# Optimization experiments

Measured on AMD Instinct MI355X. Metric: run time of the kernel, lower is better.

Reference implementation:

```python
import jax, jax.numpy as jnp
import numpy as np

N, E, G = 50000, 500000, 64
F_IN, H, C = 10, 4, 64
HC = H * C  # 256
NCLS = 8
BN_EPS = 1e-5


def _bn(x, g, b, m, v):
    # eval-mode BatchNorm1d with running stats
    return (x - m) * jax.lax.rsqrt(v + BN_EPS) * g + b


def _gat(x, src, dst, W, a_s, a_d, b):
    # PyG GATConv (concat=True): h=[N,H,C]; e_ij=leakyrelu(a_s.h_j + a_d.h_i);
    # softmax over incoming edges of each destination node; scatter-add.
    n = x.shape[0]
    h = (x @ W).reshape(n, H, C)
    es = jnp.einsum('nhc,hc->nh', h, a_s)  # source term per node
    ed = jnp.einsum('nhc,hc->nh', h, a_d)  # dest term per node
    e = jax.nn.leaky_relu(es[src] + ed[dst], 0.2)            # [E2,H]
    m = jax.ops.segment_max(e, dst, num_segments=n)
    ex = jnp.exp(e - m[dst])
    s = jax.ops.segment_sum(ex, dst, num_segments=n)
    alpha = ex / (s[dst] + 1e-16)                             # [E2,H]
    out = jax.ops.segment_sum(h[src] * alpha[:, :, None], dst, num_segments=n)
    return out.reshape(n, HC) + b, alpha


def _gcn(x, src, dst, W, b):
    n = x.shape[0]
    deg = jax.ops.segment_sum(jnp.ones_like(src, dtype=x.dtype), dst, num_segments=n)
    dinv = jax.lax.rsqrt(jnp.maximum(deg, 1.0))
    norm = dinv[src] * dinv[dst]
    xw = x @ W
    return jax.ops.segment_sum(xw[src] * norm[:, None], dst, num_segments=n) + b


def setup_inputs() -> dict:
    key = jax.random.key(0)
    ks = jax.random.split(key, 48)
    r = lambda i, sh, sc=0.1: jax.random.normal(ks[i], sh, dtype=jnp.float32) * sc
    p = {}
    p['x'] = jax.random.normal(ks[0], (N, F_IN), dtype=jnp.float32)
    p['edge_index'] = jax.random.randint(ks[1], (2, E), 0, N, dtype=jnp.int32)
    p['batch'] = jnp.sort(jax.random.randint(ks[2], (N,), 0, G, dtype=jnp.int32))
    # GAT1
    p['W1'] = r(3, (F_IN, HC)); p['as1'] = r(4, (H, C)); p['ad1'] = r(5, (H, C)); p['bi1'] = r(6, (HC,))
    # GAT2
    p['W2'] = r(7, (HC, HC)); p['as2'] = r(8, (H, C)); p['ad2'] = r(9, (H, C)); p['bi2'] = r(10, (HC,))
    # BN running stats / affine
    for i, (nm, d) in enumerate([('bn1', HC), ('bn2', HC), ('bn3', C)]):
        k0 = 11 + 4 * i
        p[nm + '_g'] = 1.0 + r(k0, (d,))
        p[nm + '_b'] = r(k0 + 1, (d,))
        p[nm + '_m'] = r(k0 + 2, (d,))
        p[nm + '_v'] = 1.0 + jax.random.uniform(ks[k0 + 3], (d,), dtype=jnp.float32) * 0.5
    # GCN
    p['Wg'] = r(23, (HC, C)); p['bg'] = r(24, (C,))
    # reduce_dim
    p['Wr'] = r(25, (2 * C, C)); p['br'] = r(26, (C,))
    # rul head
    p['Wh1'] = r(27, (C, 32)); p['bh1'] = r(28, (32,))
    p['Wh2'] = r(29, (32, 16)); p['bh2'] = r(30, (16,))
    p['Wh3'] = r(31, (16, 1)); p['bh3'] = r(32, (1,))
    # location head
    p['Wl1'] = r(33, (C, 32)); p['bl1'] = r(34, (32,))
    p['Wl2'] = r(35, (32, NCLS)); p['bl2'] = r(36, (NCLS,))
    # energy head
    p['We1'] = r(37, (C, 16)); p['be1'] = r(38, (16,))
    p['We2'] = r(39, (16, 1)); p['be2'] = r(40, (1,))
    return p


def reference(x, edge_index, batch,
              W1, as1, ad1, bi1, W2, as2, ad2, bi2,
              bn1_g, bn1_b, bn1_m, bn1_v, bn2_g, bn2_b, bn2_m, bn2_v,
              bn3_g, bn3_b, bn3_m, bn3_v,
              Wg, bg, Wr, br,
              Wh1, bh1, Wh2, bh2, Wh3, bh3,
              Wl1, bl1, Wl2, bl2, We1, be1, We2, be2):
    n = x.shape[0]
    loop = jnp.arange(n, dtype=edge_index.dtype)
    src = jnp.concatenate([edge_index[0], loop])
    dst = jnp.concatenate([edge_index[1], loop])

    h, alpha1 = _gat(x, src, dst, W1, as1, ad1, bi1)
    h = jax.nn.elu(_bn(h, bn1_g, bn1_b, bn1_m, bn1_v))  # dropout = identity (eval)
    h, alpha2 = _gat(h, src, dst, W2, as2, ad2, bi2)
    h = jax.nn.elu(_bn(h, bn2_g, bn2_b, bn2_m, bn2_v))
    h = _gcn(h, src, dst, Wg, bg)
    h = jax.nn.elu(_bn(h, bn3_g, bn3_b, bn3_m, bn3_v))  # node embeddings [N,64]

    cnt = jax.ops.segment_sum(jnp.ones((n,), h.dtype), batch, num_segments=G)
    x_mean = jax.ops.segment_sum(h, batch, num_segments=G) / jnp.maximum(cnt, 1.0)[:, None]
    x_max = jax.ops.segment_max(h, batch, num_segments=G)
    x_max = jnp.where(cnt[:, None] > 0, x_max, 0.0)
    xg = jnp.concatenate([x_mean, x_max], axis=1) @ Wr + br  # [G,64]

    t = jax.nn.relu(xg @ Wh1 + bh1)
    t = jax.nn.relu(t @ Wh2 + bh2)
    rul = jax.nn.sigmoid(t @ Wh3 + bh3) * 100.0
    loc = jax.nn.relu(xg @ Wl1 + bl1) @ Wl2 + bl2
    en = jax.nn.relu(xg @ We1 + be1) @ We2 + be2
    return rul, loc, en, h, xg
```

## Files before the change

### kernel.cpp

```cpp
#include <hip/hip_runtime.h>
#include <math.h>

#define SCAN_BLK 1024
#define BN_EPS 1e-5f

typedef __attribute__((ext_vector_type(8))) short short8;
typedef __attribute__((ext_vector_type(4))) short short4v;
typedef __attribute__((ext_vector_type(4))) float f32x4;

__device__ __forceinline__ float eluf(float x){ return x > 0.f ? x : (expf(x) - 1.f); }
__device__ __forceinline__ unsigned short f2bf(float f){
  unsigned u = __float_as_uint(f);
  u += 0x7FFFu + ((u >> 16) & 1u);
  return (unsigned short)(u >> 16);
}
__device__ __forceinline__ float bf2f(unsigned short s){
  return __uint_as_float(((unsigned)s) << 16);
}
__device__ __forceinline__ unsigned fmap(float f){
  unsigned b = __float_as_uint(f);
  return (b & 0x80000000u) ? ~b : (b | 0x80000000u);
}
__device__ __forceinline__ float funmap(unsigned u){
  unsigned b = (u & 0x80000000u) ? (u ^ 0x80000000u) : ~u;
  return __uint_as_float(b);
}

__global__ void k_count(const int* __restrict__ ei, int* __restrict__ deg, int ne, int e2)
{
  int t = blockIdx.x * 256 + threadIdx.x;
  if (t >= e2) return;
  int dst = (t < ne) ? ei[ne + t] : t - ne;
  atomicAdd(&deg[dst], 1);
}

__global__ void k_scan1(const int* __restrict__ deg, int* __restrict__ rowptr,
                        int* __restrict__ partials, int n)
{
  __shared__ int sh[SCAN_BLK];
  int t = threadIdx.x, base = blockIdx.x * SCAN_BLK;
  int v = (base + t < n) ? deg[base + t] : 0;
  sh[t] = v;
  __syncthreads();
  for (int off = 1; off < SCAN_BLK; off <<= 1) {
    int u = 0;
    if (t >= off) u = sh[t - off];
    __syncthreads();
    if (t >= off) sh[t] += u;
    __syncthreads();
  }
  if (base + t < n) rowptr[base + t] = sh[t] - v;
  if (t == SCAN_BLK - 1) partials[blockIdx.x] = sh[t];
}

__global__ void k_scan2(int* __restrict__ rowptr, const int* __restrict__ partials, int n)
{
  int base = blockIdx.x * SCAN_BLK;
  int add = 0;
  for (int i = 0; i < blockIdx.x; i++) add += partials[i];
  int t = threadIdx.x;
  if (base + t < n) rowptr[base + t] += add;
}

__global__ void k_fill(const int* __restrict__ ei, const int* __restrict__ rowptr,
                       int* __restrict__ cursor, int* __restrict__ col, int ne, int e2)
{
  int t = blockIdx.x * 256 + threadIdx.x;
  if (t >= e2) return;
  int src, dst;
  if (t < ne) { src = ei[t]; dst = ei[ne + t]; } else { src = dst = t - ne; }
  int pos = rowptr[dst] + atomicAdd(&cursor[dst], 1);
  col[pos] = src;
}

__global__ void k_dinv(const int* __restrict__ deg, float* __restrict__ dinv, int n)
{
  int t = blockIdx.x * 256 + threadIdx.x;
  if (t < n) dinv[t] = rsqrtf(fmaxf((float)deg[t], 1.f));
}

__global__ void k_pack(const float* __restrict__ W, unsigned short* __restrict__ Wp,
                       int N, int nct)
{
  int tid = threadIdx.x;
  int l = tid >> 3, j = tid & 7;
  int ct = blockIdx.x >> 3, ks = blockIdx.x & 7;
  int k = ks * 32 + (l >> 4) * 8 + j;
  int c = ct * 16 + (l & 15);
  Wp[(size_t)(ks * nct + ct) * 512 + tid] = f2bf(W[(size_t)k * N + c]);
}

__global__ void k_prep1(const float* __restrict__ W1, const float* __restrict__ as1,
                        const float* __restrict__ ad1,
                        float* __restrict__ Ws1, float* __restrict__ Wd1)
{
  int t = threadIdx.x;
  if (t >= 80) return;
  int half = t / 40, r = t % 40;
  int k = r / 4, h = r % 4;
  const float* a = half ? ad1 : as1;
  float s = 0.f;
  for (int c = 0; c < 64; c++) s += W1[k * 256 + h * 64 + c] * a[h * 64 + c];
  (half ? Wd1 : Ws1)[k * 4 + h] = s;
}

__global__ void k_prep2(const float* __restrict__ W2, const float* __restrict__ as2,
                        const float* __restrict__ ad2,
                        float* __restrict__ Was2, float* __restrict__ Wad2)
{
  int g = blockIdx.x * 256 + threadIdx.x;
  if (g >= 2048) return;
  int half = g >= 1024, r = g & 1023;
  int i = r >> 2, h = r & 3;
  const float* a = half ? ad2 : as2;
  float s = 0.f;
  for (int c = 0; c < 64; c++) s += W2[(size_t)i * 256 + h * 64 + c] * a[h * 64 + c];
  (half ? Wad2 : Was2)[i * 4 + h] = s;
}

__global__ void k_prep_bn(const float* __restrict__ bi1, const float* __restrict__ g1,
                          const float* __restrict__ b1, const float* __restrict__ m1,
                          const float* __restrict__ v1,
                          const float* __restrict__ bi2, const float* __restrict__ g2,
                          const float* __restrict__ b2, const float* __restrict__ m2,
                          const float* __restrict__ v2,
                          float* __restrict__ A1, float* __restrict__ B1,
                          float* __restrict__ A2, float* __restrict__ B2)
{
  int c = threadIdx.x;
  if (c < 256) {
    float a = rsqrtf(v1[c] + BN_EPS) * g1[c];
    A1[c] = a; B1[c] = (bi1[c] - m1[c]) * a + b1[c];
    a = rsqrtf(v2[c] + BN_EPS) * g2[c];
    A2[c] = a; B2[c] = (bi2[c] - m2[c]) * a + b2[c];
  }
}

__global__ void k_es1(const float* __restrict__ x, const float* __restrict__ Ws1,
                      const float* __restrict__ Wd1,
                      float* __restrict__ es, float* __restrict__ ed, int n)
{
  int t = blockIdx.x * 256 + threadIdx.x;
  if (t >= n) return;
  float xr[10];
  #pragma unroll
  for (int k = 0; k < 10; k++) xr[k] = x[(size_t)t * 10 + k];
  float e0[4] = {0,0,0,0}, e1[4] = {0,0,0,0};
  #pragma unroll
  for (int k = 0; k < 10; k++) {
    #pragma unroll
    for (int h = 0; h < 4; h++) {
      e0[h] += xr[k] * Ws1[k * 4 + h];
      e1[h] += xr[k] * Wd1[k * 4 + h];
    }
  }
  *(float4*)&es[t * 4] = make_float4(e0[0], e0[1], e0[2], e0[3]);
  *(float4*)&ed[t * 4] = make_float4(e1[0], e1[1], e1[2], e1[3]);
}

__global__ void k_esed2(const unsigned short* __restrict__ act,
                        const float* __restrict__ Was2, const float* __restrict__ Wad2,
                        float* __restrict__ es, float* __restrict__ ed, int n)
{
  int nn = blockIdx.x * 4 + (threadIdx.x >> 6);
  if (nn >= n) return;
  int lane = threadIdx.x & 63;
  short4v av = *(const short4v*)&act[(size_t)nn * 256 + lane * 4];
  float e0[4] = {0,0,0,0}, e1[4] = {0,0,0,0};
  #pragma unroll
  for (int j = 0; j < 4; j++) {
    int c = lane * 4 + j;
    float v = bf2f((unsigned short)av[j]);
    float4 ws = *(const float4*)&Was2[c * 4];
    float4 wd = *(const float4*)&Wad2[c * 4];
    e0[0] += v * ws.x; e0[1] += v * ws.y; e0[2] += v * ws.z; e0[3] += v * ws.w;
    e1[0] += v * wd.x; e1[1] += v * wd.y; e1[2] += v * wd.z; e1[3] += v * wd.w;
  }
  #pragma unroll
  for (int off = 1; off < 64; off <<= 1) {
    #pragma unroll
    for (int h = 0; h < 4; h++) {
      e0[h] += __shfl_xor(e0[h], off, 64);
      e1[h] += __shfl_xor(e1[h], off, 64);
    }
  }
  if (lane == 0) {
    *(float4*)&es[nn * 4] = make_float4(e0[0], e0[1], e0[2], e0[3]);
    *(float4*)&ed[nn * 4] = make_float4(e1[0], e1[1], e1[2], e1[3]);
  }
}

__global__ void k_att_ms(const int* __restrict__ rowptr, const int* __restrict__ deg,
                         const int* __restrict__ col,
                         const float* __restrict__ es, const float* __restrict__ ed,
                         float* __restrict__ alp, float* __restrict__ sinv, int n)
{
  int d = blockIdx.x * 4 + (threadIdx.x >> 6);
  if (d >= n) return;
  int lane = threadIdx.x & 63;
  int head = lane >> 4, sub = lane & 15;
  int start = rowptr[d], cnt = deg[d];
  float edh = ed[d * 4 + head];

  float m = -1e30f;
  for (int i = sub; i < cnt; i += 16) {
    int s = col[start + i];
    float a = es[s * 4 + head] + edh;
    a = a > 0.f ? a : 0.2f * a;
    m = fmaxf(m, a);
  }
  #pragma unroll
  for (int off = 1; off < 16; off <<= 1) m = fmaxf(m, __shfl_xor(m, off, 16));

  float ssum = 0.f;
  for (int i = sub; i < cnt; i += 16) {
    int s = col[start + i];
    float a = es[s * 4 + head] + edh;
    a = a > 0.f ? a : 0.2f * a;
    float ex = expf(a - m);
    alp[(size_t)(start + i) * 4 + head] = ex;
    ssum += ex;
  }
  #pragma unroll
  for (int off = 1; off < 16; off <<= 1) ssum += __shfl_xor(ssum, off, 16);
  if (sub == 0) sinv[d * 4 + head] = 1.f / (ssum + 1e-16f);
}

__global__ void k_xagg(const int* __restrict__ rowptr, const int* __restrict__ deg,
                       const int* __restrict__ col, const float* __restrict__ alp,
                       const float* __restrict__ sinv, const float* __restrict__ x,
                       float* __restrict__ xa, int n)
{
  int d = blockIdx.x * 4 + (threadIdx.x >> 6);
  if (d >= n) return;
  int lane = threadIdx.x & 63;
  int slot = lane >> 4, k = lane & 15;
  int start = rowptr[d], cnt = deg[d];
  bool active = (k < 10);

  float a0 = 0.f, a1 = 0.f, a2 = 0.f, a3 = 0.f;
  int i = slot;
  for (; i + 4 < cnt; i += 8) {
    int e0 = start + i, e1 = start + i + 4;
    int s0 = col[e0], s1 = col[e1];
    float4 al0 = *(const float4*)&alp[(size_t)e0 * 4];
    float4 al1 = *(const float4*)&alp[(size_t)e1 * 4];
    float x0 = active ? x[(size_t)s0 * 10 + k] : 0.f;
    float x1 = active ? x[(size_t)s1 * 10 + k] : 0.f;
    a0 += al0.x * x0 + al1.x * x1;
    a1 += al0.y * x0 + al1.y * x1;
    a2 += al0.z * x0 + al1.z * x1;
    a3 += al0.w * x0 + al1.w * x1;
  }
  if (i < cnt) {
    int e0 = start + i;
    int s0 = col[e0];
    float4 al0 = *(const float4*)&alp[(size_t)e0 * 4];
    float x0 = active ? x[(size_t)s0 * 10 + k] : 0.f;
    a0 += al0.x * x0; a1 += al0.y * x0; a2 += al0.z * x0; a3 += al0.w * x0;
  }
  a0 += __shfl_xor(a0, 16, 64); a0 += __shfl_xor(a0, 32, 64);
  a1 += __shfl_xor(a1, 16, 64); a1 += __shfl_xor(a1, 32, 64);
  a2 += __shfl_xor(a2, 16, 64); a2 += __shfl_xor(a2, 32, 64);
  a3 += __shfl_xor(a3, 16, 64); a3 += __shfl_xor(a3, 32, 64);

  if (slot == 0 && active) {
    float4 sv = *(const float4*)&sinv[d * 4];
    float* xo = &xa[(size_t)d * 40];
    xo[k]      = a0 * sv.x;
    xo[10 + k] = a1 * sv.y;
    xo[20 + k] = a2 * sv.z;
    xo[30 + k] = a3 * sv.w;
  }
}

__global__ void k_gemm_xa(const float* __restrict__ xa, const float* __restrict__ W1,
                          const float* __restrict__ A1, const float* __restrict__ B1,
                          unsigned short* __restrict__ actA, int n)
{
  __shared__ float xal[160];
  int tid = threadIdx.x;
  int n0 = blockIdx.x * 4;
  if (tid < 160 && (size_t)n0 * 40 + tid < (size_t)n * 40)
    xal[tid] = xa[(size_t)n0 * 40 + tid];
  __syncthreads();
  int c = tid, h = c >> 6;
  float w[10];
  #pragma unroll
  for (int k = 0; k < 10; k++) w[k] = W1[k * 256 + c];
  float a1 = A1[c], b1 = B1[c];
  #pragma unroll
  for (int m = 0; m < 4; m++) {
    int nn = n0 + m;
    if (nn >= n) break;
    float acc = 0.f;
    #pragma unroll
    for (int k = 0; k < 10; k++) acc += xal[m * 40 + h * 10 + k] * w[k];
    actA[(size_t)nn * 256 + c] = f2bf(eluf(acc * a1 + b1));
  }
}

__global__ void k_gat_gather(const int* __restrict__ rowptr, const int* __restrict__ deg,
                             const int* __restrict__ col, const float* __restrict__ alp,
                             const float* __restrict__ sinv,
                             const unsigned short* __restrict__ act,
                             unsigned short* __restrict__ outb, int n)
{
  int d = blockIdx.x * 4 + (threadIdx.x >> 6);
  if (d >= n) return;
  int lane = threadIdx.x & 63;
  int half = lane >> 5, l32 = lane & 31;
  int c8 = l32 * 8, head = l32 >> 3;
  int start = rowptr[d], cnt = deg[d];

  float acc[8] = {0.f,0.f,0.f,0.f,0.f,0.f,0.f,0.f};
  int T = (cnt > half) ? ((cnt - half + 1) >> 1) : 0;
  int ebase = start + half;
  int t = 0;
  for (; t + 4 <= T; t += 4) {
    int e0 = ebase + 2 * t, e1 = e0 + 2, e2 = e0 + 4, e3 = e0 + 6;
    int s0 = col[e0], s1 = col[e1], s2 = col[e2], s3 = col[e3];
    float a0 = alp[(size_t)e0 * 4 + head];
    float a1 = alp[(size_t)e1 * 4 + head];
    float a2 = alp[(size_t)e2 * 4 + head];
    float a3 = alp[(size_t)e3 * 4 + head];
    short8 h0 = *(const short8*)&act[(size_t)s0 * 256 + c8];
    short8 h1 = *(const short8*)&act[(size_t)s1 * 256 + c8];
    short8 h2 = *(const short8*)&act[(size_t)s2 * 256 + c8];
    short8 h3 = *(const short8*)&act[(size_t)s3 * 256 + c8];
    #pragma unroll
    for (int j = 0; j < 8; j++) {
      acc[j] += bf2f((unsigned short)h0[j]) * a0 + bf2f((unsigned short)h1[j]) * a1
              + bf2f((unsigned short)h2[j]) * a2 + bf2f((unsigned short)h3[j]) * a3;
    }
  }
  for (; t < T; t++) {
    int e0 = ebase + 2 * t;
    int s0 = col[e0];
    float a0 = alp[(size_t)e0 * 4 + head];
    short8 h0 = *(const short8*)&act[(size_t)s0 * 256 + c8];
    #pragma unroll
    for (int j = 0; j < 8; j++) acc[j] += bf2f((unsigned short)h0[j]) * a0;
  }
  #pragma unroll
  for (int j = 0; j < 8; j++)
    acc[j] += __shfl_xor(acc[j], 32, 64);

  if (half == 0) {
    float sv = sinv[d * 4 + head];
    short8 o;
    #pragma unroll
    for (int j = 0; j < 8; j++) o[j] = (short)f2bf(acc[j] * sv);
    *(short8*)&outb[(size_t)d * 256 + c8] = o;
  }
}

template<int NCT, bool BNEPI>
__global__ __launch_bounds__(256) void k_mfma_gemm(
    const unsigned short* __restrict__ act, const unsigned short* __restrict__ Wp,
    unsigned short* __restrict__ outb,
    const float* __restrict__ Abn, const float* __restrict__ Bbn, int n)
{
  __shared__ unsigned short bsh[NCT * 512];
  int tid = threadIdx.x, wave = tid >> 6, lane = tid & 63;
  int l15 = lane & 15, lg = lane >> 4;
  int rbase = blockIdx.x * 64 + wave * 16;
  int arow = rbase + l15; if (arow > n - 1) arow = n - 1;
  const unsigned short* ap = &act[(size_t)arow * 256 + lg * 8];

  constexpr int NCH = (NCT >= 4) ? NCT / 4 : 1;
  f32x4 acc[NCT];
  f32x4 z = {0.f, 0.f, 0.f, 0.f};
  #pragma unroll
  for (int ct = 0; ct < NCT; ct++) acc[ct] = z;

  for (int ks = 0; ks < 8; ks++) {
    const unsigned short* src = Wp + (size_t)ks * NCT * 512 + wave * NCT * 128;
    short8 stg[NCH];
    #pragma unroll
    for (int c = 0; c < NCH; c++)
      stg[c] = *(const short8*)(src + c * 512 + lane * 8);
    short8 a = *(const short8*)(ap + ks * 32);
    __syncthreads();
    #pragma unroll
    for (int c = 0; c < NCH; c++)
      *(short8*)&bsh[wave * NCT * 128 + c * 512 + lane * 8] = stg[c];
    __syncthreads();
    #pragma unroll
    for (int ct = 0; ct < NCT; ct++) {
      short8 b = *(const short8*)&bsh[(ct * 64 + lane) * 8];
      acc[ct] = __builtin_amdgcn_mfma_f32_16x16x32_bf16(a, b, acc[ct], 0, 0, 0);
    }
  }

  float abn[NCT], bbn[NCT];
  if (BNEPI) {
    #pragma unroll
    for (int ct = 0; ct < NCT; ct++) {
      abn[ct] = Abn[ct * 16 + l15];
      bbn[ct] = Bbn[ct * 16 + l15];
    }
  }
  #pragma unroll
  for (int r = 0; r < 4; r++) {
    int row = rbase + lg * 4 + r;
    if (row < n) {
      #pragma unroll
      for (int ct = 0; ct < NCT; ct++) {
        float v = acc[ct][r];
        if (BNEPI) v = eluf(v * abn[ct] + bbn[ct]);
        outb[(size_t)row * (NCT * 16) + ct * 16 + l15] = f2bf(v);
      }
    }
  }
}

__global__ void k_gcn_gather(const int* __restrict__ rowptr, const int* __restrict__ deg,
                             const int* __restrict__ col, const float* __restrict__ dinv,
                             const unsigned short* __restrict__ xwb,
                             const float* __restrict__ bias,
                             const float* __restrict__ gg, const float* __restrict__ bb,
                             const float* __restrict__ mm, const float* __restrict__ vv,
                             float* __restrict__ hout, int n)
{
  int d = blockIdx.x * 4 + (threadIdx.x >> 6);
  if (d >= n) return;
  int lane = threadIdx.x & 63;
  int slot = lane >> 3, cg = (lane & 7) * 8;
  int start = rowptr[d], cnt = deg[d];
  float dinvd = rsqrtf(fmaxf((float)cnt, 1.f));

  float acc[8] = {0.f,0.f,0.f,0.f,0.f,0.f,0.f,0.f};
  for (int i = slot; i < cnt; i += 8) {
    int s = col[start + i];
    float norm = dinv[s] * dinvd;
    short8 hv = *(const short8*)&xwb[(size_t)s * 64 + cg];
    #pragma unroll
    for (int j = 0; j < 8; j++)
      acc[j] += bf2f((unsigned short)hv[j]) * norm;
  }
  #pragma unroll
  for (int j = 0; j < 8; j++) {
    acc[j] += __shfl_xor(acc[j], 8, 64);
    acc[j] += __shfl_xor(acc[j], 16, 64);
    acc[j] += __shfl_xor(acc[j], 32, 64);
  }

  if (lane < 8) {
    float out[8];
    #pragma unroll
    for (int j = 0; j < 8; j++) {
      int c = cg + j;
      float r = ((acc[j] + bias[c]) - mm[c]) * rsqrtf(vv[c] + BN_EPS) * gg[c] + bb[c];
      out[j] = eluf(r);
    }
    *(float4*)&hout[(size_t)d * 64 + cg]     = make_float4(out[0], out[1], out[2], out[3]);
    *(float4*)&hout[(size_t)d * 64 + cg + 4] = make_float4(out[4], out[5], out[6], out[7]);
  }
}

__global__ void k_pool_partial(const float* __restrict__ hout, const int* __restrict__ batch,
                               float* __restrict__ psum, unsigned* __restrict__ pmaxu,
                               int n)
{
  int wave = threadIdx.x >> 6, lane = threadIdx.x & 63;
  int wbase = blockIdx.x * 128 + wave * 32;
  int wend = wbase + 32; if (wend > n) wend = n;
  if (wbase >= n) return;

  int g_cur = -1;
  float s = 0.f, mx = -1e30f;
  for (int node = wbase; node < wend; node++) {
    int g = batch[node];
    if (g != g_cur) {
      if (g_cur >= 0) {
        atomicAdd(&psum[g_cur * 64 + lane], s);
        atomicMax(&pmaxu[g_cur * 64 + lane], fmap(mx));
      }
      g_cur = g; s = 0.f; mx = -1e30f;
    }
    float v = hout[(size_t)node * 64 + lane];
    s += v;
    mx = fmaxf(mx, v);
  }
  if (g_cur >= 0) {
    atomicAdd(&psum[g_cur * 64 + lane], s);
    atomicMax(&pmaxu[g_cur * 64 + lane], fmap(mx));
  }
}

__global__ void k_heads(const float* __restrict__ psum, const unsigned* __restrict__ pmaxu,
                        const int* __restrict__ batch,
                        const float* __restrict__ Wr, const float* __restrict__ br,
                        const float* __restrict__ Wh1, const float* __restrict__ bh1,
                        const float* __restrict__ Wh2, const float* __restrict__ bh2,
                        const float* __restrict__ Wh3, const float* __restrict__ bh3,
                        const float* __restrict__ Wl1, const float* __restrict__ bl1,
                        const float* __restrict__ Wl2, const float* __restrict__ bl2,
                        const float* __restrict__ We1, const float* __restrict__ be1,
                        const float* __restrict__ We2, const float* __restrict__ be2,
                        float* __restrict__ outp, int n, int xg_off)
{
  __shared__ float cat[128], xg[64], t1[32], t2[16], l1[32], e1[16];
  int g = blockIdx.x, c = threadIdx.x;

  int lo = 0, hi = n;
  while (lo < hi) { int mid = (lo + hi) >> 1; if (batch[mid] < g) lo = mid + 1; else hi = mid; }
  int start = lo;
  lo = start; hi = n;
  while (lo < hi) { int mid = (lo + hi) >> 1; if (batch[mid] < g + 1) lo = mid + 1; else hi = mid; }
  int cntg = lo - start;

  float mean = psum[g * 64 + c] / fmaxf((float)cntg, 1.f);
  float mxv = (cntg > 0) ? funmap(pmaxu[g * 64 + c]) : 0.f;
  cat[c] = mean; cat[64 + c] = mxv;
  __syncthreads();
  float a = br[c];
  for (int i = 0; i < 128; i++) a += cat[i] * Wr[i * 64 + c];
  xg[c] = a;
  outp[xg_off + g * 64 + c] = a;
  __syncthreads();
  if (c < 32) {
    float u = bh1[c]; for (int i = 0; i < 64; i++) u += xg[i] * Wh1[i * 32 + c];
    t1[c] = fmaxf(u, 0.f);
    float v = bl1[c]; for (int i = 0; i < 64; i++) v += xg[i] * Wl1[i * 32 + c];
    l1[c] = fmaxf(v, 0.f);
  }
  __syncthreads();
  if (c < 16) {
    float u = bh2[c]; for (int i = 0; i < 32; i++) u += t1[i] * Wh2[i * 16 + c];
    t2[c] = fmaxf(u, 0.f);
    float v = be1[c]; for (int i = 0; i < 64; i++) v += xg[i] * We1[i * 16 + c];
    e1[c] = fmaxf(v, 0.f);
  }
  __syncthreads();
  if (c < 8) {
    float v = bl2[c]; for (int i = 0; i < 32; i++) v += l1[i] * Wl2[i * 8 + c];
    outp[64 + g * 8 + c] = v;
  }
  if (c == 0) {
    float u = bh3[0]; for (int i = 0; i < 16; i++) u += t2[i] * Wh3[i];
    outp[g] = 100.f / (1.f + expf(-u));
    float v = be2[0]; for (int i = 0; i < 16; i++) v += e1[i] * We2[i];
    outp[576 + g] = v;
  }
}

extern "C" void kernel_launch(void* const* d_in, const int* in_sizes, int n_in,
                              void* d_out, int out_size, void* d_ws, size_t ws_size,
                              hipStream_t stream)
{
  const float* x    = (const float*)d_in[0];
  const int*   ei   = (const int*)d_in[1];
  const int*   batch= (const int*)d_in[2];
  const float* W1   = (const float*)d_in[3];
  const float* as1  = (const float*)d_in[4];
  const float* ad1  = (const float*)d_in[5];
  const float* bi1  = (const float*)d_in[6];
  const float* W2   = (const float*)d_in[7];
  const float* as2  = (const float*)d_in[8];
  const float* ad2  = (const float*)d_in[9];
  const float* bi2  = (const float*)d_in[10];
  const float* bn1g = (const float*)d_in[11];
  const float* bn1b = (const float*)d_in[12];
  const float* bn1m = (const float*)d_in[13];
  const float* bn1v = (const float*)d_in[14];
  const float* bn2g = (const float*)d_in[15];
  const float* bn2b = (const float*)d_in[16];
  const float* bn2m = (const float*)d_in[17];
  const float* bn2v = (const float*)d_in[18];
  const float* bn3g = (const float*)d_in[19];
  const float* bn3b = (const float*)d_in[20];
  const float* bn3m = (const float*)d_in[21];
  const float* bn3v = (const float*)d_in[22];
  const float* Wg   = (const float*)d_in[23];
  const float* bg   = (const float*)d_in[24];
  const float* Wr   = (const float*)d_in[25];
  const float* br   = (const float*)d_in[26];
  const float* Wh1  = (const float*)d_in[27];
  const float* bh1  = (const float*)d_in[28];
  const float* Wh2  = (const float*)d_in[29];
  const float* bh2  = (const float*)d_in[30];
  const float* Wh3  = (const float*)d_in[31];
  const float* bh3  = (const float*)d_in[32];
  const float* Wl1  = (const float*)d_in[33];
  const float* bl1  = (const float*)d_in[34];
  const float* Wl2  = (const float*)d_in[35];
  const float* bl2  = (const float*)d_in[36];
  const float* We1  = (const float*)d_in[37];
  const float* be1  = (const float*)d_in[38];
  const float* We2  = (const float*)d_in[39];
  const float* be2  = (const float*)d_in[40];

  const int n  = in_sizes[2];
  const int ne = in_sizes[1] / 2;
  const int e2 = ne + n;

  float* ws = (float*)d_ws;
  size_t off = 0;
  unsigned short* bufA = (unsigned short*)(ws + off); off += (size_t)n * 128;
  unsigned short* bufB = (unsigned short*)(ws + off); off += (size_t)n * 128;
  float* xa   = ws + off; off += (size_t)n * 40;
  float* es   = ws + off; off += (size_t)n * 4;
  float* ed   = ws + off; off += (size_t)n * 4;
  float* alp  = ws + off; off += (size_t)e2 * 4;
  float* sinv = ws + off; off += (size_t)n * 4;
  float* dinv = ws + off; off += (size_t)n;
  int* rowptr = (int*)(ws + off); off += (size_t)n + 1;
  int* deg    = (int*)(ws + off); off += (size_t)n;
  int* cursor = (int*)(ws + off); off += (size_t)n;
  int* col    = (int*)(ws + off); off += (size_t)e2;
  int* partials = (int*)(ws + off); off += 64;
  unsigned short* Wp2 = (unsigned short*)(ws + off); off += 32768;
  unsigned short* Wpg = (unsigned short*)(ws + off); off += 8192;
  float* Ws1  = ws + off; off += 40;
  float* Wd1  = ws + off; off += 40;
  float* Was2 = ws + off; off += 1024;
  float* Wad2 = ws + off; off += 1024;
  float* A1   = ws + off; off += 256;
  float* B1   = ws + off; off += 256;
  float* A2   = ws + off; off += 256;
  float* B2   = ws + off; off += 256;
  float* psum = ws + off; off += 64 * 64;
  unsigned* pmaxu = (unsigned*)(ws + off); off += 64 * 64;

  unsigned short* actA = bufA;
  unsigned short* agg2 = bufB;
  unsigned short* actB = bufA;
  unsigned short* xwb  = bufB;

  float* outp = (float*)d_out;
  float* hout = outp + 640;
  const int xg_off = 640 + n * 64;

  const int eb   = (e2 + 255) / 256;
  const int gb1  = (n + 3) / 4;
  const int gmb  = (n + 63) / 64;
  const int nsb  = (n + SCAN_BLK - 1) / SCAN_BLK;

  hipMemsetAsync(deg, 0, (size_t)n * sizeof(int), stream);
  hipMemsetAsync(cursor, 0, (size_t)n * sizeof(int), stream);
  k_count<<<eb, 256, 0, stream>>>(ei, deg, ne, e2);
  k_scan1<<<nsb, SCAN_BLK, 0, stream>>>(deg, rowptr, partials, n);
  k_scan2<<<nsb, SCAN_BLK, 0, stream>>>(rowptr, partials, n);
  k_fill<<<eb, 256, 0, stream>>>(ei, rowptr, cursor, col, ne, e2);
  k_dinv<<<(n + 255) / 256, 256, 0, stream>>>(deg, dinv, n);
  k_pack<<<128, 512, 0, stream>>>(W2, Wp2, 256, 16);
  k_pack<<<32, 512, 0, stream>>>(Wg, Wpg, 64, 4);
  k_prep1<<<1, 128, 0, stream>>>(W1, as1, ad1, Ws1, Wd1);
  k_prep2<<<8, 256, 0, stream>>>(W2, as2, ad2, Was2, Wad2);
  k_prep_bn<<<1, 256, 0, stream>>>(bi1, bn1g, bn1b, bn1m, bn1v,
                                   bi2, bn2g, bn2b, bn2m, bn2v,
                                   A1, B1, A2, B2);

  k_es1<<<(n + 255) / 256, 256, 0, stream>>>(x, Ws1, Wd1, es, ed, n);
  k_att_ms<<<gb1, 256, 0, stream>>>(rowptr, deg, col, es, ed, alp, sinv, n);
  k_xagg<<<gb1, 256, 0, stream>>>(rowptr, deg, col, alp, sinv, x, xa, n);
  k_gemm_xa<<<gb1, 256, 0, stream>>>(xa, W1, A1, B1, actA, n);

  k_esed2<<<gb1, 256, 0, stream>>>(actA, Was2, Wad2, es, ed, n);
  k_att_ms<<<gb1, 256, 0, stream>>>(rowptr, deg, col, es, ed, alp, sinv, n);
  k_gat_gather<<<gb1, 256, 0, stream>>>(rowptr, deg, col, alp, sinv, actA, agg2, n);
  k_mfma_gemm<16, true><<<gmb, 256, 0, stream>>>(agg2, Wp2, actB, A2, B2, n);

  k_mfma_gemm<4, false><<<gmb, 256, 0, stream>>>(actB, Wpg, xwb, nullptr, nullptr, n);
  k_gcn_gather<<<gb1, 256, 0, stream>>>(rowptr, deg, col, dinv, xwb,
                                        bg, bn3g, bn3b, bn3m, bn3v, hout, n);

  hipMemsetAsync(psum, 0, 64 * 64 * sizeof(float), stream);
  hipMemsetAsync(pmaxu, 0, 64 * 64 * sizeof(unsigned), stream);
  k_pool_partial<<<(n + 127) / 128, 256, 0, stream>>>(hout, batch, psum, pmaxu, n);
  k_heads<<<64, 64, 0, stream>>>(psum, pmaxu, batch, Wr, br,
                                 Wh1, bh1, Wh2, bh2, Wh3, bh3,
                                 Wl1, bl1, Wl2, bl2, We1, be1, We2, be2,
                                 outp, n, xg_off);
}
```

Baseline: 342.6 us.

## Fuse attention softmax into gather kernels, drop max subtraction and alpha buffer

Removes the separate attention kernel that computed per-edge exponentials and inverse sums. Both GAT aggregation kernels now recompute exp(leakyrelu(es+ed)) inline and accumulate the normalising sum themselves. This removes a full edge pass and the per-edge alpha write and read. The softmax no longer subtracts the per-destination max, which risks overflow when logits are large. The esed2 kernel is also restructured to 8 threads per node with transposed weights, and the GCN gather is unrolled by two with dinv[dst] hoisted out of the loop.

```diff
diff --git a/kernel.cpp b/kernel.cpp
--- a/kernel.cpp
+++ b/kernel.cpp
@@ -25,6 +25,7 @@
   unsigned b = (u & 0x80000000u) ? (u ^ 0x80000000u) : ~u;
   return __uint_as_float(b);
 }
+__device__ __forceinline__ float lrelu(float a){ return a > 0.f ? a : 0.2f * a; }
 
 __global__ void k_count(const int* __restrict__ ei, int* __restrict__ deg, int ne, int e2)
 {
@@ -105,8 +106,7 @@
 }
 
 __global__ void k_prep2(const float* __restrict__ W2, const float* __restrict__ as2,
-                        const float* __restrict__ ad2,
-                        float* __restrict__ Was2, float* __restrict__ Wad2)
+                        const float* __restrict__ ad2, float* __restrict__ WasT)
 {
   int g = blockIdx.x * 256 + threadIdx.x;
   if (g >= 2048) return;
@@ -115,7 +115,7 @@
   const float* a = half ? ad2 : as2;
   float s = 0.f;
   for (int c = 0; c < 64; c++) s += W2[(size_t)i * 256 + h * 64 + c] * a[h * 64 + c];
-  (half ? Wad2 : Was2)[i * 4 + h] = s;
+  WasT[(size_t)(half * 4 + h) * 256 + i] = s;
 }
 
 __global__ void k_prep_bn(const float* __restrict__ bi1, const float* __restrict__ g1,
@@ -159,77 +159,33 @@
 }
 
 __global__ void k_esed2(const unsigned short* __restrict__ act,
-                        const float* __restrict__ Was2, const float* __restrict__ Wad2,
+                        const float* __restrict__ WasT,
                         float* __restrict__ es, float* __restrict__ ed, int n)
 {
-  int nn = blockIdx.x * 4 + (threadIdx.x >> 6);
+  int t = blockIdx.x * 256 + threadIdx.x;
+  int nn = t >> 3, q = t & 7;
   if (nn >= n) return;
-  int lane = threadIdx.x & 63;
-  short4v av = *(const short4v*)&act[(size_t)nn * 256 + lane * 4];
-  float e0[4] = {0,0,0,0}, e1[4] = {0,0,0,0};
-  #pragma unroll
-  for (int j = 0; j < 4; j++) {
-    int c = lane * 4 + j;
-    float v = bf2f((unsigned short)av[j]);
-    float4 ws = *(const float4*)&Was2[c * 4];
-    float4 wd = *(const float4*)&Wad2[c * 4];
-    e0[0] += v * ws.x; e0[1] += v * ws.y; e0[2] += v * ws.z; e0[3] += v * ws.w;
-    e1[0] += v * wd.x; e1[1] += v * wd.y; e1[2] += v * wd.z; e1[3] += v * wd.w;
-  }
-  #pragma unroll
-  for (int off = 1; off < 64; off <<= 1) {
-    #pragma unroll
-    for (int h = 0; h < 4; h++) {
-      e0[h] += __shfl_xor(e0[h], off, 64);
-      e1[h] += __shfl_xor(e1[h], off, 64);
-    }
-  }
-  if (lane == 0) {
-    *(float4*)&es[nn * 4] = make_float4(e0[0], e0[1], e0[2], e0[3]);
-    *(float4*)&ed[nn * 4] = make_float4(e1[0], e1[1], e1[2], e1[3]);
-  }
-}
-
-__global__ void k_att_ms(const int* __restrict__ rowptr, const int* __restrict__ deg,
-                         const int* __restrict__ col,
-                         const float* __restrict__ es, const float* __restrict__ ed,
-                         float* __restrict__ alp, float* __restrict__ sinv, int n)
-{
-  int d = blockIdx.x * 4 + (threadIdx.x >> 6);
-  if (d >= n) return;
-  int lane = threadIdx.x & 63;
-  int head = lane >> 4, sub = lane & 15;
-  int start = rowptr[d], cnt = deg[d];
-  float edh = ed[d * 4 + head];
-
-  float m = -1e30f;
-  for (int i = sub; i < cnt; i += 16) {
-    int s = col[start + i];
-    float a = es[s * 4 + head] + edh;
-    a = a > 0.f ? a : 0.2f * a;
-    m = fmaxf(m, a);
-  }
-  #pragma unroll
-  for (int off = 1; off < 16; off <<= 1) m = fmaxf(m, __shfl_xor(m, off, 16));
-
-  float ssum = 0.f;
-  for (int i = sub; i < cnt; i += 16) {
-    int s = col[start + i];
-    float a = es[s * 4 + head] + edh;
-    a = a > 0.f ? a : 0.2f * a;
-    float ex = expf(a - m);
-    alp[(size_t)(start + i) * 4 + head] = ex;
-    ssum += ex;
-  }
-  #pragma unroll
-  for (int off = 1; off < 16; off <<= 1) ssum += __shfl_xor(ssum, off, 16);
-  if (sub == 0) sinv[d * 4 + head] = 1.f / (ssum + 1e-16f);
+  const unsigned short* ar = &act[(size_t)nn * 256];
+  const float* wr = &WasT[(size_t)q * 256];
+  float s = 0.f;
+  #pragma unroll 4
+  for (int c0 = 0; c0 < 256; c0 += 8) {
+    short8 av = *(const short8*)(ar + c0);
+    float4 w0 = *(const float4*)(wr + c0);
+    float4 w1 = *(const float4*)(wr + c0 + 4);
+    s += bf2f((unsigned short)av[0]) * w0.x + bf2f((unsigned short)av[1]) * w0.y
+       + bf2f((unsigned short)av[2]) * w0.z + bf2f((unsigned short)av[3]) * w0.w
+       + bf2f((unsigned short)av[4]) * w1.x + bf2f((unsigned short)av[5]) * w1.y
+       + bf2f((unsigned short)av[6]) * w1.z + bf2f((unsigned short)av[7]) * w1.w;
+  }
+  if (q < 4) es[nn * 4 + q] = s;
+  else       ed[nn * 4 + (q - 4)] = s;
 }
 
 __global__ void k_xagg(const int* __restrict__ rowptr, const int* __restrict__ deg,
-                       const int* __restrict__ col, const float* __restrict__ alp,
-                       const float* __restrict__ sinv, const float* __restrict__ x,
-                       float* __restrict__ xa, int n)
+                       const int* __restrict__ col,
+                       const float* __restrict__ es, const float* __restrict__ ed,
+                       const float* __restrict__ x, float* __restrict__ xa, int n)
 {
   int d = blockIdx.x * 4 + (threadIdx.x >> 6);
   if (d >= n) return;
@@ -237,40 +193,54 @@
   int slot = lane >> 4, k = lane & 15;
   int start = rowptr[d], cnt = deg[d];
   bool active = (k < 10);
+  float4 edv = *(const float4*)&ed[d * 4];
 
   float a0 = 0.f, a1 = 0.f, a2 = 0.f, a3 = 0.f;
+  float s0 = 0.f, s1 = 0.f, s2 = 0.f, s3 = 0.f;
   int i = slot;
   for (; i + 4 < cnt; i += 8) {
     int e0 = start + i, e1 = start + i + 4;
-    int s0 = col[e0], s1 = col[e1];
-    float4 al0 = *(const float4*)&alp[(size_t)e0 * 4];
-    float4 al1 = *(const float4*)&alp[(size_t)e1 * 4];
-    float x0 = active ? x[(size_t)s0 * 10 + k] : 0.f;
-    float x1 = active ? x[(size_t)s1 * 10 + k] : 0.f;
-    a0 += al0.x * x0 + al1.x * x1;
-    a1 += al0.y * x0 + al1.y * x1;
-    a2 += al0.z * x0 + al1.z * x1;
-    a3 += al0.w * x0 + al1.w * x1;
+    int sa = col[e0], sb = col[e1];
+    float4 u0 = *(const float4*)&es[sa * 4];
+    float4 u1 = *(const float4*)&es[sb * 4];
+    float x0 = active ? x[(size_t)sa * 10 + k] : 0.f;
+    float x1 = active ? x[(size_t)sb * 10 + k] : 0.f;
+    float ex;
+    ex = expf(lrelu(u0.x + edv.x)); a0 += ex * x0; s0 += ex;
+    ex = expf(lrelu(u0.y + edv.y)); a1 += ex * x0; s1 += ex;
+    ex = expf(lrelu(u0.z + edv.z)); a2 += ex * x0; s2 += ex;
+    ex = expf(lrelu(u0.w + edv.w)); a3 += ex * x0; s3 += ex;
+    ex = expf(lrelu(u1.x + edv.x)); a0 += ex * x1; s0 += ex;
+    ex = expf(lrelu(u1.y + edv.y)); a1 += ex * x1; s1 += ex;
+    ex = expf(lrelu(u1.z + edv.z)); a2 += ex * x1; s2 += ex;
+    ex = expf(lrelu(u1.w + edv.w)); a3 += ex * x1; s3 += ex;
   }
   if (i < cnt) {
     int e0 = start + i;
-    int s0 = col[e0];
-    float4 al0 = *(const float4*)&alp[(size_t)e0 * 4];
-    float x0 = active ? x[(size_t)s0 * 10 + k] : 0.f;
-    a0 += al0.x * x0; a1 += al0.y * x0; a2 += al0.z * x0; a3 += al0.w * x0;
+    int sa = col[e0];
+    float4 u0 = *(const float4*)&es[sa * 4];
+    float x0 = active ? x[(size_t)sa * 10 + k] : 0.f;
+    float ex;
+    ex = expf(lrelu(u0.x + edv.x)); a0 += ex * x0; s0 += ex;
+    ex = expf(lrelu(u0.y + edv.y)); a1 += ex * x0; s1 += ex;
+    ex = expf(lrelu(u0.z + edv.z)); a2 += ex * x0; s2 += ex;
+    ex = expf(lrelu(u0.w + edv.w)); a3 += ex * x0; s3 += ex;
   }
   a0 += __shfl_xor(a0, 16, 64); a0 += __shfl_xor(a0, 32, 64);
   a1 += __shfl_xor(a1, 16, 64); a1 += __shfl_xor(a1, 32, 64);
   a2 += __shfl_xor(a2, 16, 64); a2 += __shfl_xor(a2, 32, 64);
   a3 += __shfl_xor(a3, 16, 64); a3 += __shfl_xor(a3, 32, 64);
+  s0 += __shfl_xor(s0, 16, 64); s0 += __shfl_xor(s0, 32, 64);
+  s1 += __shfl_xor(s1, 16, 64); s1 += __shfl_xor(s1, 32, 64);
+  s2 += __shfl_xor(s2, 16, 64); s2 += __shfl_xor(s2, 32, 64);
+  s3 += __shfl_xor(s3, 16, 64); s3 += __shfl_xor(s3, 32, 64);
 
   if (slot == 0 && active) {
-    float4 sv = *(const float4*)&sinv[d * 4];
     float* xo = &xa[(size_t)d * 40];
-    xo[k]      = a0 * sv.x;
-    xo[10 + k] = a1 * sv.y;
-    xo[20 + k] = a2 * sv.z;
-    xo[30 + k] = a3 * sv.w;
+    xo[k]      = a0 / (s0 + 1e-16f);
+    xo[10 + k] = a1 / (s1 + 1e-16f);
+    xo[20 + k] = a2 / (s2 + 1e-16f);
+    xo[30 + k] = a3 / (s3 + 1e-16f);
   }
 }
 
@@ -301,8 +271,8 @@
 }
 
 __global__ void k_gat_gather(const int* __restrict__ rowptr, const int* __restrict__ deg,
-                             const int* __restrict__ col, const float* __restrict__ alp,
-                             const float* __restrict__ sinv,
+                             const int* __restrict__ col,
+                             const float* __restrict__ es, const float* __restrict__ ed,
                              const unsigned short* __restrict__ act,
                              unsigned short* __restrict__ outb, int n)
 {
@@ -312,42 +282,47 @@
   int half = lane >> 5, l32 = lane & 31;
   int c8 = l32 * 8, head = l32 >> 3;
   int start = rowptr[d], cnt = deg[d];
+  float edh = ed[d * 4 + head];
 
   float acc[8] = {0.f,0.f,0.f,0.f,0.f,0.f,0.f,0.f};
+  float sex = 0.f;
   int T = (cnt > half) ? ((cnt - half + 1) >> 1) : 0;
   int ebase = start + half;
   int t = 0;
   for (; t + 4 <= T; t += 4) {
     int e0 = ebase + 2 * t, e1 = e0 + 2, e2 = e0 + 4, e3 = e0 + 6;
     int s0 = col[e0], s1 = col[e1], s2 = col[e2], s3 = col[e3];
-    float a0 = alp[(size_t)e0 * 4 + head];
-    float a1 = alp[(size_t)e1 * 4 + head];
-    float a2 = alp[(size_t)e2 * 4 + head];
-    float a3 = alp[(size_t)e3 * 4 + head];
+    float x0 = expf(lrelu(es[s0 * 4 + head] + edh));
+    float x1 = expf(lrelu(es[s1 * 4 + head] + edh));
+    float x2 = expf(lrelu(es[s2 * 4 + head] + edh));
+    float x3 = expf(lrelu(es[s3 * 4 + head] + edh));
     short8 h0 = *(const short8*)&act[(size_t)s0 * 256 + c8];
     short8 h1 = *(const short8*)&act[(size_t)s1 * 256 + c8];
     short8 h2 = *(const short8*)&act[(size_t)s2 * 256 + c8];
     short8 h3 = *(const short8*)&act[(size_t)s3 * 256 + c8];
     #pragma unroll
     for (int j = 0; j < 8; j++) {
-      acc[j] += bf2f((unsigned short)h0[j]) * a0 + bf2f((unsigned short)h1[j]) * a1
-              + bf2f((unsigned short)h2[j]) * a2 + bf2f((unsigned short)h3[j]) * a3;
+      acc[j] += bf2f((unsigned short)h0[j]) * x0 + bf2f((unsigned short)h1[j]) * x1
+              + bf2f((unsigned short)h2[j]) * x2 + bf2f((unsigned short)h3[j]) * x3;
     }
+    sex += x0 + x1 + x2 + x3;
   }
   for (; t < T; t++) {
     int e0 = ebase + 2 * t;
     int s0 = col[e0];
-    float a0 = alp[(size_t)e0 * 4 + head];
+    float x0 = expf(lrelu(es[s0 * 4 + head] + edh));
     short8 h0 = *(const short8*)&act[(size_t)s0 * 256 + c8];
     #pragma unroll
-    for (int j = 0; j < 8; j++) acc[j] += bf2f((unsigned short)h0[j]) * a0;
+    for (int j = 0; j < 8; j++) acc[j] += bf2f((unsigned short)h0[j]) * x0;
+    sex += x0;
   }
   #pragma unroll
   for (int j = 0; j < 8; j++)
     acc[j] += __shfl_xor(acc[j], 32, 64);
+  sex += __shfl_xor(sex, 32, 64);
 
   if (half == 0) {
-    float sv = sinv[d * 4 + head];
+    float sv = 1.f / (sex + 1e-16f);
     short8 o;
     #pragma unroll
     for (int j = 0; j < 8; j++) o[j] = (short)f2bf(acc[j] * sv);
@@ -431,19 +406,30 @@
   float dinvd = rsqrtf(fmaxf((float)cnt, 1.f));
 
   float acc[8] = {0.f,0.f,0.f,0.f,0.f,0.f,0.f,0.f};
-  for (int i = slot; i < cnt; i += 8) {
-    int s = col[start + i];
-    float norm = dinv[s] * dinvd;
-    short8 hv = *(const short8*)&xwb[(size_t)s * 64 + cg];
+  int i = slot;
+  for (; i + 8 < cnt; i += 16) {
+    int s0 = col[start + i], s1 = col[start + i + 8];
+    float n0 = dinv[s0], n1 = dinv[s1];
+    short8 h0 = *(const short8*)&xwb[(size_t)s0 * 64 + cg];
+    short8 h1 = *(const short8*)&xwb[(size_t)s1 * 64 + cg];
     #pragma unroll
     for (int j = 0; j < 8; j++)
-      acc[j] += bf2f((unsigned short)hv[j]) * norm;
+      acc[j] += bf2f((unsigned short)h0[j]) * n0 + bf2f((unsigned short)h1[j]) * n1;
+  }
+  if (i < cnt) {
+    int s0 = col[start + i];
+    float n0 = dinv[s0];
+    short8 h0 = *(const short8*)&xwb[(size_t)s0 * 64 + cg];
+    #pragma unroll
+    for (int j = 0; j < 8; j++)
+      acc[j] += bf2f((unsigned short)h0[j]) * n0;
   }
   #pragma unroll
   for (int j = 0; j < 8; j++) {
     acc[j] += __shfl_xor(acc[j], 8, 64);
     acc[j] += __shfl_xor(acc[j], 16, 64);
     acc[j] += __shfl_xor(acc[j], 32, 64);
+    acc[j] *= dinvd;
   }
 
   if (lane < 8) {
@@ -603,8 +589,6 @@
   float* xa   = ws + off; off += (size_t)n * 40;
   float* es   = ws + off; off += (size_t)n * 4;
   float* ed   = ws + off; off += (size_t)n * 4;
-  float* alp  = ws + off; off += (size_t)e2 * 4;
-  float* sinv = ws + off; off += (size_t)n * 4;
   float* dinv = ws + off; off += (size_t)n;
   int* rowptr = (int*)(ws + off); off += (size_t)n + 1;
   int* deg    = (int*)(ws + off); off += (size_t)n;
@@ -615,8 +599,7 @@
   unsigned short* Wpg = (unsigned short*)(ws + off); off += 8192;
   float* Ws1  = ws + off; off += 40;
   float* Wd1  = ws + off; off += 40;
-  float* Was2 = ws + off; off += 1024;
-  float* Wad2 = ws + off; off += 1024;
+  float* WasT = ws + off; off += 2048;
   float* A1   = ws + off; off += 256;
   float* B1   = ws + off; off += 256;
   float* A2   = ws + off; off += 256;
@@ -648,19 +631,17 @@
   k_pack<<<128, 512, 0, stream>>>(W2, Wp2, 256, 16);
   k_pack<<<32, 512, 0, stream>>>(Wg, Wpg, 64, 4);
   k_prep1<<<1, 128, 0, stream>>>(W1, as1, ad1, Ws1, Wd1);
-  k_prep2<<<8, 256, 0, stream>>>(W2, as2, ad2, Was2, Wad2);
+  k_prep2<<<8, 256, 0, stream>>>(W2, as2, ad2, WasT);
   k_prep_bn<<<1, 256, 0, stream>>>(bi1, bn1g, bn1b, bn1m, bn1v,
                                    bi2, bn2g, bn2b, bn2m, bn2v,
                                    A1, B1, A2, B2);
 
   k_es1<<<(n + 255) / 256, 256, 0, stream>>>(x, Ws1, Wd1, es, ed, n);
-  k_att_ms<<<gb1, 256, 0, stream>>>(rowptr, deg, col, es, ed, alp, sinv, n);
-  k_xagg<<<gb1, 256, 0, stream>>>(rowptr, deg, col, alp, sinv, x, xa, n);
+  k_xagg<<<gb1, 256, 0, stream>>>(rowptr, deg, col, es, ed, x, xa, n);
   k_gemm_xa<<<gb1, 256, 0, stream>>>(xa, W1, A1, B1, actA, n);
 
-  k_esed2<<<gb1, 256, 0, stream>>>(actA, Was2, Wad2, es, ed, n);
-  k_att_ms<<<gb1, 256, 0, stream>>>(rowptr, deg, col, es, ed, alp, sinv, n);
-  k_gat_gather<<<gb1, 256, 0, stream>>>(rowptr, deg, col, alp, sinv, actA, agg2, n);
+  k_esed2<<<(n * 8 + 255) / 256, 256, 0, stream>>>(actA, WasT, es, ed, n);
+  k_gat_gather<<<gb1, 256, 0, stream>>>(rowptr, deg, col, es, ed, actA, agg2, n);
   k_mfma_gemm<16, true><<<gmb, 256, 0, stream>>>(agg2, Wp2, actB, A2, B2, n);
 
   k_mfma_gemm<4, false><<<gmb, 256, 0, stream>>>(actB, Wpg, xwb, nullptr, nullptr, n);
```

Measured after the change: 343.9 us. About the same (+0.4%).
